# Performance work log

Hardware: AMD Instinct MI355X
Metric: run time of the kernel (lower is better)

## Reference

```python
import jax, jax.numpy as jnp
import numpy as np
from jax import lax

D_MODEL = 768
N_LAYER = 4
D_STATE = 16
D_CONV = 4
EXPAND = 2
VOCAB = 32000
B = 1
L = 1024
D_INNER = D_MODEL * EXPAND
EPS = 1e-5


def setup_inputs() -> dict:
    key = jax.random.key(0)
    ks = jax.random.split(key, 8)
    s = 0.02
    A_row = jnp.log(jnp.arange(1, D_STATE + 1, dtype=jnp.float32))  # log(1..N)
    return {
        "idx": jax.random.randint(ks[0], (B, L), 0, VOCAB),
        "embed": jax.random.normal(ks[1], (VOCAB, D_MODEL), jnp.float32) * s,
        "norm_w": jnp.ones((N_LAYER, D_MODEL), jnp.float32),
        "W_in": jax.random.normal(ks[2], (N_LAYER, 2 * D_INNER, D_MODEL), jnp.float32) * s,
        "conv_w": jax.random.normal(ks[3], (N_LAYER, D_INNER, 1, D_CONV), jnp.float32) * s,
        "conv_b": jnp.zeros((N_LAYER, D_INNER), jnp.float32),
        "W_x": jax.random.normal(ks[4], (N_LAYER, 2 * D_STATE + 1, D_INNER), jnp.float32) * s,
        "dt_w": jax.random.normal(ks[5], (N_LAYER, D_INNER, 1), jnp.float32) * s,
        "dt_b": jnp.zeros((N_LAYER, D_INNER), jnp.float32),
        "A_log": jnp.tile(A_row, (N_LAYER, D_INNER, 1)),
        "Dp": jnp.ones((N_LAYER, D_INNER), jnp.float32),
        "out_w": jax.random.normal(ks[6], (N_LAYER, D_MODEL, D_INNER), jnp.float32) * s,
        "norm_f_w": jnp.ones((D_MODEL,), jnp.float32),
    }


def rmsnorm(x, w):
    return x / jnp.sqrt(jnp.mean(x * x, axis=-1, keepdims=True) + EPS) * w


def selective_scan(xc, W_x, dt_w, dt_b, A_log, Dp):
    # xc: [B, L, D_INNER]
    A = -jnp.exp(A_log)                               # [D, N]
    xp = xc @ W_x.T                                   # [B, L, 2N+1]
    dt_r = xp[..., :1]
    Bv = xp[..., 1:1 + D_STATE]                       # [B, L, N]
    Cv = xp[..., 1 + D_STATE:]                        # [B, L, N]
    dt = jax.nn.softplus(dt_r * dt_w[:, 0] + dt_b)    # [B, L, D]
    dA = jnp.exp(dt[..., None] * A)                   # [B, L, D, N]
    dBx = dt[..., None] * Bv[:, :, None, :] * xc[..., None]  # [B, L, D, N]

    def step(h, inp):
        dA_t, dBx_t, C_t = inp
        h = dA_t * h + dBx_t                          # [B, D, N]
        y = jnp.einsum('bdn,bn->bd', h, C_t)          # [B, D]
        return h, y

    h0 = jnp.zeros((xc.shape[0], D_INNER, D_STATE), xc.dtype)
    _, ys = lax.scan(step, h0, (dA.transpose(1, 0, 2, 3),
                                dBx.transpose(1, 0, 2, 3),
                                Cv.transpose(1, 0, 2)))
    return ys.transpose(1, 0, 2) + xc * Dp            # [B, L, D]


def mamba_block(x, W_in, conv_w, conv_b, W_x, dt_w, dt_b, A_log, Dp, out_w):
    xz = x @ W_in.T                                   # [B, L, 2*D_INNER]
    x_ssm, z = jnp.split(xz, 2, axis=-1)
    # depthwise causal conv1d (torch pads both sides then keeps first L == left pad only)
    xc = lax.conv_general_dilated(x_ssm.transpose(0, 2, 1), conv_w, (1,),
                                  [(D_CONV - 1, 0)],
                                  feature_group_count=D_INNER,
                                  dimension_numbers=('NCH', 'OIH', 'NCH'))
    xc = (xc + conv_b[None, :, None]).transpose(0, 2, 1)
    xc = jax.nn.silu(xc)
    y = selective_scan(xc, W_x, dt_w, dt_b, A_log, Dp)
    y = y * jax.nn.silu(z)
    return y @ out_w.T


def reference(idx, embed, norm_w, W_in, conv_w, conv_b, W_x, dt_w, dt_b, A_log, Dp, out_w, norm_f_w):
    x = embed[idx]  # dropout in eval mode == identity
    for i in range(N_LAYER):
        x = x + mamba_block(rmsnorm(x, norm_w[i]), W_in[i], conv_w[i], conv_b[i],
                            W_x[i], dt_w[i], dt_b[i], A_log[i], Dp[i], out_w[i])
    x = rmsnorm(x, norm_f_w)
    logits = x @ embed.T  # tied lm_head
    return logits
```

## Files before the change

kernel.cpp:

```cpp
#include <hip/hip_runtime.h>

#define D_MODEL 768
#define D_INNER 1536
#define D_XZ    3072
#define D_STATE 16
#define LSEQ    1024
#define NCHUNK  32
#define CLEN    32

typedef float  floatx4 __attribute__((ext_vector_type(4)));
typedef __bf16 bf16x2  __attribute__((ext_vector_type(2)));
typedef __bf16 bf16x8  __attribute__((ext_vector_type(8)));

__device__ __forceinline__ float softplus_f(float x) {
  float e = __expf(-fabsf(x));
  return fmaxf(x, 0.f) + __logf(1.f + e);
}
__device__ __forceinline__ float silu_f(float x) {
  return x / (1.f + __expf(-x));
}
__device__ __forceinline__ void gload_lds16(const void* g, void* l) {
  __builtin_amdgcn_global_load_lds(
      (const __attribute__((address_space(1))) void*)g,
      (__attribute__((address_space(3))) void*)l, 16, 0, 0);
}

template <int N> __device__ __forceinline__ void waitcnt_vm() {
  asm volatile("s_waitcnt vmcnt(%0)" ::"n"(N) : "memory");
}
__device__ __forceinline__ void cfence() { asm volatile("" ::: "memory"); }

__global__ __launch_bounds__(256) void k_cvt(const float* __restrict__ src,
                                             __bf16* __restrict__ dst) {
  size_t i = ((size_t)blockIdx.x * 256 + threadIdx.x) * 8;
  float4 a = *(const float4*)(src + i);
  float4 b = *(const float4*)(src + i + 4);
  bf16x8 o;
  o[0] = (__bf16)a.x; o[1] = (__bf16)a.y; o[2] = (__bf16)a.z; o[3] = (__bf16)a.w;
  o[4] = (__bf16)b.x; o[5] = (__bf16)b.y; o[6] = (__bf16)b.z; o[7] = (__bf16)b.w;
  *(bf16x8*)(dst + i) = o;
}

__global__ __launch_bounds__(256) void k_gather(const float* __restrict__ embed,
                                                const int* __restrict__ idx,
                                                float* __restrict__ x) {
  int t = blockIdx.x;
  int tok = idx[t];
  const float* src = embed + (size_t)tok * D_MODEL;
  float* dst = x + (size_t)t * D_MODEL;
  for (int c = threadIdx.x; c < D_MODEL; c += 256) dst[c] = src[c];
}

__global__ __launch_bounds__(256) void k_rmsnorm_bf(const float* __restrict__ x,
                                                    const float* __restrict__ w,
                                                    __bf16* __restrict__ o) {
  int lane = threadIdx.x & 63;
  int row = blockIdx.x * 4 + (threadIdx.x >> 6);
  const float* xr = x + (size_t)row * D_MODEL;
  float2 v[6];
  float ss = 0.f;
#pragma unroll
  for (int i = 0; i < 6; i++) {
    v[i] = *(const float2*)(xr + lane * 2 + i * 128);
    ss += v[i].x * v[i].x + v[i].y * v[i].y;
  }
#pragma unroll
  for (int m = 32; m; m >>= 1) ss += __shfl_xor(ss, m, 64);
  float r = rsqrtf(ss * (1.f / 768.f) + 1e-5f);
  __bf16* orow = o + (size_t)row * D_MODEL;
#pragma unroll
  for (int i = 0; i < 6; i++) {
    float2 wv = *(const float2*)(w + lane * 2 + i * 128);
    bf16x2 p;
    p[0] = (__bf16)(v[i].x * r * wv.x);
    p[1] = (__bf16)(v[i].y * r * wv.y);
    *(bf16x2*)(orow + lane * 2 + i * 128) = p;
  }
}

template <int TM, int TN>
__global__ __launch_bounds__(256) void k_gemm_bb(const __bf16* __restrict__ A,
                                                 const __bf16* __restrict__ B,
                                                 const float* res, float* __restrict__ C,
                                                 int M, int N, int K, int mTiles) {
  constexpr int MT  = TM / 32;
  constexpr int NTL = TN / 32;
  constexpr int NLA = TM / 64;
  constexpr int NLB = TN / 64;
  constexpr int NL  = NLA + NLB;
  __shared__ __attribute__((aligned(16))) __bf16 As[4][TM * 32];
  __shared__ __attribute__((aligned(16))) __bf16 Bs[4][TN * 32];
  const int tid = threadIdx.x;
  const int lane = tid & 63, wave = tid >> 6;
  const int fr = lane & 15, q = lane >> 4;

  int id = blockIdx.x;
  int per = gridDim.x >> 3;
  int v = (id & 7) * per + (id >> 3);
  int nt = v / mTiles, mt_ = v % mTiles;
  const int Mblk = mt_ * TM, Nblk = nt * TN;
  const int wm = (wave & 1) * (TM / 2), wn = (wave >> 1) * (TN / 2);

  const int row_s = tid >> 2;
  const int cs = ((tid & 3) ^ ((row_s >> 1) & 3)) * 8;
  const __bf16* Ag = A + (size_t)(Mblk + row_s) * K + cs;
  const __bf16* Bg = B + (size_t)(Nblk + row_s) * K + cs;

  floatx4 acc[MT][NTL];
#pragma unroll
  for (int i = 0; i < MT; i++)
#pragma unroll
    for (int j = 0; j < NTL; j++) {
      floatx4 z = {0.f, 0.f, 0.f, 0.f};
      acc[i][j] = z;
    }

  const int KT = K >> 5;

#define STAGE_T(t)                                                            \
  do {                                                                        \
    const int _b = (t) & 3;                                                   \
    const int _k0 = (t) << 5;                                                 \
    _Pragma("unroll") for (int i = 0; i < NLA; i++)                           \
        gload_lds16(Ag + (size_t)(64 * i) * K + _k0,                          \
                    &As[_b][tid * 8 + i * 2048]);                             \
    _Pragma("unroll") for (int i = 0; i < NLB; i++)                           \
        gload_lds16(Bg + (size_t)(64 * i) * K + _k0,                          \
                    &Bs[_b][tid * 8 + i * 2048]);                             \
  } while (0)

#define STEP_T(kt, WN)                                                        \
  do {                                                                        \
    const int _cur = (kt) & 3;                                                \
    waitcnt_vm<WN>();                                                         \
    __builtin_amdgcn_s_barrier();          \
    cfence();                                                                 \
    bf16x8 af[MT], bfr[NTL];                                                  \
    _Pragma("unroll") for (int mt = 0; mt < MT; mt++) {                       \
      const int R = wm + mt * 16 + fr;                                        \
      af[mt] = *(const bf16x8*)&As[_cur][R * 32 + ((q ^ ((R >> 1) & 3)) << 3)]; \
    }                                                                         \
    _Pragma("unroll") for (int ntl = 0; ntl < NTL; ntl++) {                   \
      const int R = wn + ntl * 16 + fr;                                       \
      bfr[ntl] = *(const bf16x8*)&Bs[_cur][R * 32 + ((q ^ ((R >> 1) & 3)) << 3)]; \
    }                                                                         \
    _Pragma("unroll") for (int mt = 0; mt < MT; mt++)                         \
      _Pragma("unroll") for (int ntl = 0; ntl < NTL; ntl++)                   \
        acc[mt][ntl] = __builtin_amdgcn_mfma_f32_16x16x32_bf16(               \
            af[mt], bfr[ntl], acc[mt][ntl], 0, 0, 0);                         \
    cfence();                                                                 \
    __builtin_amdgcn_s_barrier();              \
    cfence();                                                                 \
  } while (0)

  STAGE_T(0);
  STAGE_T(1);
  STAGE_T(2);

  int kt = 0;
  for (; kt < KT - 3; ++kt) {
    STAGE_T(kt + 3);
    STEP_T(kt, 3 * NL);
  }
  STEP_T(kt, 2 * NL); ++kt;
  STEP_T(kt, 1 * NL); ++kt;
  STEP_T(kt, 0);

#undef STAGE_T
#undef STEP_T

#pragma unroll
  for (int mt = 0; mt < MT; mt++)
#pragma unroll
    for (int ntl = 0; ntl < NTL; ntl++) {
      int r = Mblk + wm + mt * 16 + (lane >> 4) * 4;
      int c = Nblk + wn + ntl * 16 + fr;
#pragma unroll
      for (int i = 0; i < 4; i++) {
        size_t o = (size_t)(r + i) * N + c;
        float vv = acc[mt][ntl][i];
        if (res) vv += res[o];
        C[o] = vv;
      }
    }
}

__global__ __launch_bounds__(256) void k_xpconv(const float* __restrict__ xz,
                                                const float* __restrict__ cw4,
                                                const float* __restrict__ cb,
                                                const float* __restrict__ Wx,
                                                float* __restrict__ xc,
                                                float* __restrict__ xp) {
  __shared__ float red[4][33];
  int t = blockIdx.x;
  int wave = threadIdx.x >> 6, lane = threadIdx.x & 63;
  float acc[33];
#pragma unroll
  for (int j = 0; j < 33; j++) acc[j] = 0.f;
  for (int ii = 0; ii < 6; ii++) {
    int k = wave * 384 + ii * 64 + lane;
    float4 w = *(const float4*)(cw4 + (size_t)k * 4);
    float wv[4] = {w.x, w.y, w.z, w.w};
    float vv = cb[k];
#pragma unroll
    for (int jj = 0; jj < 4; jj++) {
      int ts = t - 3 + jj;
      if (ts >= 0) vv += wv[jj] * xz[(size_t)ts * D_XZ + k];
    }
    float xcv = silu_f(vv);
    xc[(size_t)t * D_INNER + k] = xcv;
#pragma unroll
    for (int j = 0; j < 33; j++) acc[j] += xcv * Wx[(size_t)j * D_INNER + k];
  }
#pragma unroll
  for (int j = 0; j < 33; j++) {
    float s = acc[j];
#pragma unroll
    for (int m = 32; m; m >>= 1) s += __shfl_xor(s, m, 64);
    if (lane == j) red[wave][j] = s;
  }
  __syncthreads();
  int j = threadIdx.x;
  if (j < 33) xp[(size_t)t * 33 + j] = red[0][j] + red[1][j] + red[2][j] + red[3][j];
}

__global__ __launch_bounds__(256) void k_scan1(const float* __restrict__ xp,
                                               const float* __restrict__ xc,
                                               const float* __restrict__ dtw,
                                               const float* __restrict__ dtb,
                                               const float* __restrict__ Alog,
                                               float* __restrict__ hend,
                                               float* __restrict__ Pp) {
  __shared__ float sxp[CLEN * 33];
  int c = blockIdx.x;
  int d = blockIdx.y * 256 + threadIdx.x;
  for (int i = threadIdx.x; i < CLEN * 33; i += 256) sxp[i] = xp[(size_t)c * CLEN * 33 + i];
  __syncthreads();
  float Av[16];
#pragma unroll
  for (int n = 0; n < 16; n++) Av[n] = -__expf(Alog[(size_t)d * 16 + n]);
  float w_ = dtw[d], b_ = dtb[d];
  float h[16], P[16];
#pragma unroll
  for (int n = 0; n < 16; n++) { h[n] = 0.f; P[n] = 1.f; }
  const float* xcc = xc + (size_t)(c * CLEN) * D_INNER + d;
  for (int tl = 0; tl < CLEN; tl++) {
    float dtr = sxp[tl * 33];
    float xv = xcc[(size_t)tl * D_INNER];
    float dt = softplus_f(dtr * w_ + b_);
    float sx = dt * xv;
#pragma unroll
    for (int n = 0; n < 16; n++) {
      float dA = __expf(dt * Av[n]);
      h[n] = dA * h[n] + sx * sxp[tl * 33 + 1 + n];
      P[n] *= dA;
    }
  }
  size_t o = ((size_t)c * D_INNER + d) * 16;
#pragma unroll
  for (int n = 0; n < 16; n++) { hend[o + n] = h[n]; Pp[o + n] = P[n]; }
}

__global__ __launch_bounds__(256) void k_scan2(const float* __restrict__ xp,
                                               const float* __restrict__ xc,
                                               const float* __restrict__ xz,
                                               const float* __restrict__ dtw,
                                               const float* __restrict__ dtb,
                                               const float* __restrict__ Alog,
                                               const float* __restrict__ Dp,
                                               const float* __restrict__ hend,
                                               const float* __restrict__ Pp,
                                               __bf16* __restrict__ g) {
  __shared__ float sxp[CLEN * 33];
  int c = blockIdx.x;
  int d = blockIdx.y * 256 + threadIdx.x;
  for (int i = threadIdx.x; i < CLEN * 33; i += 256) sxp[i] = xp[(size_t)c * CLEN * 33 + i];
  __syncthreads();
  float Av[16];
#pragma unroll
  for (int n = 0; n < 16; n++) Av[n] = -__expf(Alog[(size_t)d * 16 + n]);
  float w_ = dtw[d], b_ = dtb[d], Dv = Dp[d];
  float h[16];
#pragma unroll
  for (int n = 0; n < 16; n++) h[n] = 0.f;
  for (int c2 = 0; c2 < c; c2++) {
    size_t o = ((size_t)c2 * D_INNER + d) * 16;
#pragma unroll
    for (int n4 = 0; n4 < 4; n4++) {
      float4 hv = *(const float4*)(hend + o + n4 * 4);
      float4 pv = *(const float4*)(Pp + o + n4 * 4);
      h[n4 * 4 + 0] = pv.x * h[n4 * 4 + 0] + hv.x;
      h[n4 * 4 + 1] = pv.y * h[n4 * 4 + 1] + hv.y;
      h[n4 * 4 + 2] = pv.z * h[n4 * 4 + 2] + hv.z;
      h[n4 * 4 + 3] = pv.w * h[n4 * 4 + 3] + hv.w;
    }
  }
  for (int tl = 0; tl < CLEN; tl++) {
    int t = c * CLEN + tl;
    float dtr = sxp[tl * 33];
    float xv = xc[(size_t)t * D_INNER + d];
    float dt = softplus_f(dtr * w_ + b_);
    float sx = dt * xv;
    float y = 0.f;
#pragma unroll
    for (int n = 0; n < 16; n++) {
      float dA = __expf(dt * Av[n]);
      h[n] = dA * h[n] + sx * sxp[tl * 33 + 1 + n];
      y += h[n] * sxp[tl * 33 + 17 + n];
    }
    float z = xz[(size_t)t * D_XZ + D_INNER + d];
    g[(size_t)t * D_INNER + d] = (__bf16)((y + xv * Dv) * silu_f(z));
  }
}

extern "C" void kernel_launch(void* const* d_in, const int* in_sizes, int n_in,
                              void* d_out, int out_size, void* d_ws, size_t ws_size,
                              hipStream_t stream) {
  const int*   idx     = (const int*)d_in[0];
  const float* embed   = (const float*)d_in[1];
  const float* norm_w  = (const float*)d_in[2];
  const float* W_in    = (const float*)d_in[3];
  const float* conv_w  = (const float*)d_in[4];
  const float* conv_b  = (const float*)d_in[5];
  const float* W_x     = (const float*)d_in[6];
  const float* dt_w    = (const float*)d_in[7];
  const float* dt_b    = (const float*)d_in[8];
  const float* A_log   = (const float*)d_in[9];
  const float* Dp      = (const float*)d_in[10];
  const float* out_w   = (const float*)d_in[11];
  const float* norm_fw = (const float*)d_in[12];
  float* out = (float*)d_out;

  float*  x    = (float*)d_ws;
  __bf16* xnb  = (__bf16*)(x + 786432);
  float*  xp   = (float*)(xnb + 786432);
  float*  Pp   = xp + 33792;
  __bf16* gbf  = (__bf16*)(Pp + 786432);
  __bf16* pool = gbf + 1572864;
  __bf16* W_in_bf  = pool;
  __bf16* out_w_bf = pool + 9437184;
  float*  xz   = (float*)(out_w_bf + 4718592);
  float*  xc   = xz + 3145728;
  float*  hend = xc + 1572864;
  __bf16* emb_bf = pool;

  k_cvt<<<4608, 256, 0, stream>>>(W_in, W_in_bf);
  k_cvt<<<2304, 256, 0, stream>>>(out_w, out_w_bf);

  k_gather<<<1024, 256, 0, stream>>>(embed, idx, x);

  for (int l = 0; l < 4; l++) {
    k_rmsnorm_bf<<<256, 256, 0, stream>>>(x, norm_w + (size_t)l * D_MODEL, xnb);
    k_gemm_bb<64, 128><<<384, 256, 0, stream>>>(xnb, W_in_bf + (size_t)l * D_XZ * D_MODEL,
                                                nullptr, xz, 1024, D_XZ, D_MODEL, 16);
    k_xpconv<<<1024, 256, 0, stream>>>(xz, conv_w + (size_t)l * D_INNER * 4,
                                       conv_b + (size_t)l * D_INNER,
                                       W_x + (size_t)l * 33 * D_INNER, xc, xp);
    k_scan1<<<dim3(NCHUNK, 6), 256, 0, stream>>>(xp, xc, dt_w + (size_t)l * D_INNER,
                                                 dt_b + (size_t)l * D_INNER,
                                                 A_log + (size_t)l * D_INNER * 16, hend, Pp);
    k_scan2<<<dim3(NCHUNK, 6), 256, 0, stream>>>(xp, xc, xz, dt_w + (size_t)l * D_INNER,
                                                 dt_b + (size_t)l * D_INNER,
                                                 A_log + (size_t)l * D_INNER * 16,
                                                 Dp + (size_t)l * D_INNER, hend, Pp, gbf);
    k_gemm_bb<64, 64><<<192, 256, 0, stream>>>(gbf, out_w_bf + (size_t)l * D_MODEL * D_INNER,
                                               x, x, 1024, D_MODEL, D_INNER, 16);
  }

  k_cvt<<<12000, 256, 0, stream>>>(embed, emb_bf);
  k_rmsnorm_bf<<<256, 256, 0, stream>>>(x, norm_fw, xnb);
  k_gemm_bb<128, 128><<<2000, 256, 0, stream>>>(xnb, emb_bf, nullptr, out,
                                                1024, 32000, D_MODEL, 8);
}
```

Measured before the change: 873.6 us.

## Add split-K to out-proj GEMM, shrink in-proj tiles, use triple-buffered LDS

The GEMM kernel gains a split-K template parameter. The out-projection GEMM now splits K four ways into partial buffers (reusing the xz scratch), and a new reduction kernel adds the partials into the residual. The in-projection GEMM uses 64x64 tiles with twice as many blocks, and the pipeline drops from 4 to 3 LDS buffers with a launch-bounds occupancy hint of 3. These changes aim to fill more CUs for the small GEMMs, at the cost of an extra kernel launch, extra partial-sum memory traffic, and a shallower prefetch depth.

```diff
diff --git a/kernel.cpp b/kernel.cpp
--- a/kernel.cpp
+++ b/kernel.cpp
@@ -78,18 +78,18 @@
   }
 }
 
-template <int TM, int TN>
-__global__ __launch_bounds__(256) void k_gemm_bb(const __bf16* __restrict__ A,
-                                                 const __bf16* __restrict__ B,
-                                                 const float* res, float* __restrict__ C,
-                                                 int M, int N, int K, int mTiles) {
+template <int TM, int TN, int SK>
+__global__ __launch_bounds__(256, 3) void k_gemm_bb(const __bf16* __restrict__ A,
+                                                    const __bf16* __restrict__ B,
+                                                    const float* res, float* __restrict__ C,
+                                                    int M, int N, int K, int mTiles) {
   constexpr int MT  = TM / 32;
   constexpr int NTL = TN / 32;
   constexpr int NLA = TM / 64;
   constexpr int NLB = TN / 64;
   constexpr int NL  = NLA + NLB;
-  __shared__ __attribute__((aligned(16))) __bf16 As[4][TM * 32];
-  __shared__ __attribute__((aligned(16))) __bf16 Bs[4][TN * 32];
+  __shared__ __attribute__((aligned(16))) __bf16 As[3][TM * 32];
+  __shared__ __attribute__((aligned(16))) __bf16 Bs[3][TN * 32];
   const int tid = threadIdx.x;
   const int lane = tid & 63, wave = tid >> 6;
   const int fr = lane & 15, q = lane >> 4;
@@ -97,14 +97,18 @@
   int id = blockIdx.x;
   int per = gridDim.x >> 3;
   int v = (id & 7) * per + (id >> 3);
-  int nt = v / mTiles, mt_ = v % mTiles;
+  int s = 0, rr = v;
+  if (SK > 1) { int perS = gridDim.x / SK; s = v / perS; rr = v % perS; }
+  int nt = rr / mTiles, mt_ = rr % mTiles;
   const int Mblk = mt_ * TM, Nblk = nt * TN;
   const int wm = (wave & 1) * (TM / 2), wn = (wave >> 1) * (TN / 2);
+  const int Ks = K / SK;
 
   const int row_s = tid >> 2;
   const int cs = ((tid & 3) ^ ((row_s >> 1) & 3)) * 8;
-  const __bf16* Ag = A + (size_t)(Mblk + row_s) * K + cs;
-  const __bf16* Bg = B + (size_t)(Nblk + row_s) * K + cs;
+  const __bf16* Ag = A + (size_t)(Mblk + row_s) * K + (size_t)s * Ks + cs;
+  const __bf16* Bg = B + (size_t)(Nblk + row_s) * K + (size_t)s * Ks + cs;
+  if (SK > 1) C += (size_t)s * M * N;
 
   floatx4 acc[MT][NTL];
 #pragma unroll
@@ -115,34 +119,32 @@
       acc[i][j] = z;
     }
 
-  const int KT = K >> 5;
-
-#define STAGE_T(t)                                                            \
+  const int KT = Ks >> 5;
+
+#define STAGE_T(t, b)                                                         \
   do {                                                                        \
-    const int _b = (t) & 3;                                                   \
     const int _k0 = (t) << 5;                                                 \
     _Pragma("unroll") for (int i = 0; i < NLA; i++)                           \
         gload_lds16(Ag + (size_t)(64 * i) * K + _k0,                          \
-                    &As[_b][tid * 8 + i * 2048]);                             \
+                    &As[b][tid * 8 + i * 2048]);                              \
     _Pragma("unroll") for (int i = 0; i < NLB; i++)                           \
         gload_lds16(Bg + (size_t)(64 * i) * K + _k0,                          \
-                    &Bs[_b][tid * 8 + i * 2048]);                             \
+                    &Bs[b][tid * 8 + i * 2048]);                              \
   } while (0)
 
-#define STEP_T(kt, WN)                                                        \
+#define STEP_T(b, WN)                                                         \
   do {                                                                        \
-    const int _cur = (kt) & 3;                                                \
     waitcnt_vm<WN>();                                                         \
-    __builtin_amdgcn_s_barrier();          \
+    __builtin_amdgcn_s_barrier();     \
     cfence();                                                                 \
     bf16x8 af[MT], bfr[NTL];                                                  \
     _Pragma("unroll") for (int mt = 0; mt < MT; mt++) {                       \
       const int R = wm + mt * 16 + fr;                                        \
-      af[mt] = *(const bf16x8*)&As[_cur][R * 32 + ((q ^ ((R >> 1) & 3)) << 3)]; \
+      af[mt] = *(const bf16x8*)&As[b][R * 32 + ((q ^ ((R >> 1) & 3)) << 3)];  \
     }                                                                         \
     _Pragma("unroll") for (int ntl = 0; ntl < NTL; ntl++) {                   \
       const int R = wn + ntl * 16 + fr;                                       \
-      bfr[ntl] = *(const bf16x8*)&Bs[_cur][R * 32 + ((q ^ ((R >> 1) & 3)) << 3)]; \
+      bfr[ntl] = *(const bf16x8*)&Bs[b][R * 32 + ((q ^ ((R >> 1) & 3)) << 3)]; \
     }                                                                         \
     _Pragma("unroll") for (int mt = 0; mt < MT; mt++)                         \
       _Pragma("unroll") for (int ntl = 0; ntl < NTL; ntl++)                   \
@@ -153,18 +155,19 @@
     cfence();                                                                 \
   } while (0)
 
-  STAGE_T(0);
-  STAGE_T(1);
-  STAGE_T(2);
-
-  int kt = 0;
-  for (; kt < KT - 3; ++kt) {
-    STAGE_T(kt + 3);
-    STEP_T(kt, 3 * NL);
-  }
-  STEP_T(kt, 2 * NL); ++kt;
-  STEP_T(kt, 1 * NL); ++kt;
-  STEP_T(kt, 0);
+  STAGE_T(0, 0);
+  STAGE_T(1, 1);
+
+  int bcur = 0, bpre = 2;
+  for (int kt = 0; kt < KT - 2; ++kt) {
+    STAGE_T(kt + 2, bpre);
+    STEP_T(bcur, 2 * NL);
+    bcur = (bcur == 2) ? 0 : bcur + 1;
+    bpre = (bpre == 2) ? 0 : bpre + 1;
+  }
+  STEP_T(bcur, NL);
+  bcur = (bcur == 2) ? 0 : bcur + 1;
+  STEP_T(bcur, 0);
 
 #undef STAGE_T
 #undef STEP_T
@@ -173,7 +176,7 @@
   for (int mt = 0; mt < MT; mt++)
 #pragma unroll
     for (int ntl = 0; ntl < NTL; ntl++) {
-      int r = Mblk + wm + mt * 16 + (lane >> 4) * 4;
+      int r = Mblk + wm + mt * 16 + q * 4;
       int c = Nblk + wn + ntl * 16 + fr;
 #pragma unroll
       for (int i = 0; i < 4; i++) {
@@ -183,6 +186,21 @@
         C[o] = vv;
       }
     }
+}
+
+__global__ __launch_bounds__(256) void k_redK(const float* __restrict__ p,
+                                              float* __restrict__ x) {
+  size_t i = ((size_t)blockIdx.x * 256 + threadIdx.x) * 4;
+  float4 a  = *(float4*)(x + i);
+  float4 p0 = *(const float4*)(p + i);
+  float4 p1 = *(const float4*)(p + 786432 + i);
+  float4 p2 = *(const float4*)(p + 2 * 786432 + i);
+  float4 p3 = *(const float4*)(p + 3 * 786432 + i);
+  a.x += ((p0.x + p1.x) + p2.x) + p3.x;
+  a.y += ((p0.y + p1.y) + p2.y) + p3.y;
+  a.z += ((p0.z + p1.z) + p2.z) + p3.z;
+  a.w += ((p0.w + p1.w) + p2.w) + p3.w;
+  *(float4*)(x + i) = a;
 }
 
 __global__ __launch_bounds__(256) void k_xpconv(const float* __restrict__ xz,
@@ -351,8 +369,8 @@
 
   for (int l = 0; l < 4; l++) {
     k_rmsnorm_bf<<<256, 256, 0, stream>>>(x, norm_w + (size_t)l * D_MODEL, xnb);
-    k_gemm_bb<64, 128><<<384, 256, 0, stream>>>(xnb, W_in_bf + (size_t)l * D_XZ * D_MODEL,
-                                                nullptr, xz, 1024, D_XZ, D_MODEL, 16);
+    k_gemm_bb<64, 64, 1><<<768, 256, 0, stream>>>(xnb, W_in_bf + (size_t)l * D_XZ * D_MODEL,
+                                                  nullptr, xz, 1024, D_XZ, D_MODEL, 16);
     k_xpconv<<<1024, 256, 0, stream>>>(xz, conv_w + (size_t)l * D_INNER * 4,
                                        conv_b + (size_t)l * D_INNER,
                                        W_x + (size_t)l * 33 * D_INNER, xc, xp);
@@ -363,12 +381,13 @@
                                                  dt_b + (size_t)l * D_INNER,
                                                  A_log + (size_t)l * D_INNER * 16,
                                                  Dp + (size_t)l * D_INNER, hend, Pp, gbf);
-    k_gemm_bb<64, 64><<<192, 256, 0, stream>>>(gbf, out_w_bf + (size_t)l * D_MODEL * D_INNER,
-                                               x, x, 1024, D_MODEL, D_INNER, 16);
+    k_gemm_bb<64, 64, 4><<<768, 256, 0, stream>>>(gbf, out_w_bf + (size_t)l * D_MODEL * D_INNER,
+                                                  nullptr, xz, 1024, D_MODEL, D_INNER, 16);
+    k_redK<<<768, 256, 0, stream>>>(xz, x);
   }
 
   k_cvt<<<12000, 256, 0, stream>>>(embed, emb_bf);
   k_rmsnorm_bf<<<256, 256, 0, stream>>>(x, norm_fw, xnb);
-  k_gemm_bb<128, 128><<<2000, 256, 0, stream>>>(xnb, emb_bf, nullptr, out,
-                                                1024, 32000, D_MODEL, 8);
-}
+  k_gemm_bb<128, 128, 1><<<2000, 256, 0, stream>>>(xnb, emb_bf, nullptr, out,
+                                                   1024, 32000, D_MODEL, 8);
+}
```

Measured after the change: 823.6 us. 1.06x faster.
